# Kernel tuning notes

Hardware: AMD Instinct MI355X
Metric: run time of the kernel (lower is better)

The kernel has to match this reference:

```python
import jax, jax.numpy as jnp
import numpy as np
from jax import lax

NPOINT = 1024
K = 32
EPS = 1e-5  # BatchNorm2d default eps


def setup_inputs() -> dict:
    key = jax.random.key(0)
    ks = jax.random.split(key, 8)
    B, N = 16, 4096
    xyz = jax.random.normal(ks[0], (B, N, 3), dtype=jnp.float32)
    init_farthest = jax.random.randint(ks[1], (B,), 0, N, dtype=jnp.int32)
    def w(k, o, i):
        return jax.random.normal(k, (o, i), dtype=jnp.float32) * (1.0 / np.sqrt(i))
    chans = [3, 64, 64, 128]
    inp = {"xyz": xyz, "init_farthest": init_farthest}
    for li in range(3):
        ci, co = chans[li], chans[li + 1]
        inp[f"W{li+1}"] = w(ks[2 + li], co, ci)
        inp[f"b{li+1}"] = jnp.zeros((co,), jnp.float32)
        inp[f"g{li+1}"] = jnp.ones((co,), jnp.float32)
        inp[f"be{li+1}"] = jnp.zeros((co,), jnp.float32)
    return inp


def _farthest_point_sample(xyz, init_farthest, npoint):
    # Sequential FPS: npoint iterations of distance-update + argmax (lax.scan).
    B, N, _ = xyz.shape
    bidx = jnp.arange(B)
    def step(carry, _):
        distance, farthest = carry
        centroid = xyz[bidx, farthest][:, None, :]            # [B,1,3]
        d = jnp.sum((xyz - centroid) ** 2, axis=-1)           # [B,N]
        distance = jnp.minimum(distance, d)
        return (distance, jnp.argmax(distance, axis=-1)), farthest
    init = (jnp.full((B, N), 1e10, xyz.dtype), init_farthest)
    _, centroids = lax.scan(step, init, None, length=npoint)  # [npoint,B]
    return centroids.T                                        # [B,npoint]


def _forward(xyz, init_farthest, params):
    B, N, _ = xyz.shape
    fps_idx = _farthest_point_sample(xyz, init_farthest, NPOINT)      # [B,S]
    bidx = jnp.arange(B)[:, None]
    new_xyz = xyz[bidx, fps_idx]                                       # [B,S,3]
    # KNN over sampled points (pairwise squared distances, [B,S,S])
    dist = jnp.sum((new_xyz[:, :, None, :] - new_xyz[:, None, :, :]) ** 2, axis=-1)
    idx = jnp.argsort(dist, axis=-1)[:, :, 1:K + 1]                    # [B,S,K]
    # NOTE: faithful to original code: idx (values < npoint) indexes xyz rows.
    grouped = xyz[jnp.arange(B)[:, None, None], idx]                   # [B,S,K,3]
    grouped = grouped - new_xyz[:, :, None, :]
    x = jnp.transpose(grouped, (0, 3, 1, 2))                           # [B,3,S,K]
    for (W, b, g, be) in params:
        x = jnp.einsum('oc,bcsk->bosk', W, x) + b[None, :, None, None]
        m = x.mean(axis=(0, 2, 3), keepdims=True)
        v = x.var(axis=(0, 2, 3), keepdims=True)                       # biased var (BN train mode)
        x = g[None, :, None, None] * (x - m) * lax.rsqrt(v + EPS) + be[None, :, None, None]
        x = jax.nn.relu(x)
    new_points = jnp.max(x, axis=-1)                                   # [B,128,S]
    return new_xyz, new_points


def reference(xyz, init_farthest, W1, b1, g1, be1, W2, b2, g2, be2, W3, b3, g3, be3):
    params = [(W1, b1, g1, be1), (W2, b2, g2, be2), (W3, b3, g3, be3)]
    return _forward(xyz, init_farthest, params)
```

## Files before the change

kernel.cpp:

```cpp
#include <hip/hip_runtime.h>


#define Bc 16
#define Nn 4096
#define Ss 1024
#define Kk 32
#define COLS (Bc*Ss*Kk)
#define EPSF 1e-5f

#define S2SUM 16
#define S2SQ  528
#define S3SUM 1040
#define S3SQ  2064

typedef unsigned long long ull;
typedef unsigned int uint32;

__device__ __forceinline__ unsigned short f2bf(float f){
  uint32 u = __float_as_uint(f);
  uint32 r = (u + 0x7fffu + ((u>>16)&1u)) >> 16;
  return (unsigned short)r;
}
__device__ __forceinline__ float bf2f(unsigned short h){ return __uint_as_float(((uint32)h)<<16); }

__device__ __forceinline__ float dppmax_f32(float x){
  #define STEPF(ctrl,rm) { int _s=__builtin_amdgcn_update_dpp(__float_as_int(x),__float_as_int(x),(ctrl),(rm),0xf,false); x=fmaxf(x,__int_as_float(_s)); }
  STEPF(0x111,0xf) STEPF(0x112,0xf) STEPF(0x114,0xf) STEPF(0x118,0xf)
  STEPF(0x142,0xa) STEPF(0x143,0xc)
  #undef STEPF
  return __int_as_float(__builtin_amdgcn_readlane(__float_as_int(x),63));
}
__device__ __forceinline__ int dppmin_i32(int x){
  #define STEPI(ctrl,rm) { int _s=__builtin_amdgcn_update_dpp(x,x,(ctrl),(rm),0xf,false); x=min(x,_s); }
  STEPI(0x111,0xf) STEPI(0x112,0xf) STEPI(0x114,0xf) STEPI(0x118,0xf)
  STEPI(0x142,0xa) STEPI(0x143,0xc)
  #undef STEPI
  return __builtin_amdgcn_readlane(x,63);
}

__global__ __launch_bounds__(256) void fps_kernel(const float* __restrict__ xyz,
                                                  const int* __restrict__ init_far,
                                                  float* __restrict__ new_xyz){
  __shared__ float sx[Nn*4];
  __shared__ ull wk[2][4];
  int b = blockIdx.x, t = threadIdx.x;
  int lane = t & 63, wid = t >> 6;
  const float* xb = xyz + (size_t)b*Nn*3;
  const float4* xb4 = (const float4*)xb;
  for(int i=t;i<Nn*3/4;i+=256){
    float4 v = xb4[i];
    int f0 = 4*i;
    sx[(f0/3)*4 + (f0%3)]       = v.x;
    sx[((f0+1)/3)*4 + ((f0+1)%3)] = v.y;
    sx[((f0+2)/3)*4 + ((f0+2)%3)] = v.z;
    sx[((f0+3)/3)*4 + ((f0+3)%3)] = v.w;
  }
  __syncthreads();
  const float4* sxp = (const float4*)sx;
  float px[16],py[16],pz[16],dd[16];
  #pragma unroll
  for(int j=0;j<16;j++){ int n=t+256*j; float4 p=sxp[n]; px[j]=p.x; py[j]=p.y; pz[j]=p.z; dd[j]=1e10f; }
  int far = init_far[b];
  float o0x=0.f,o0y=0.f,o0z=0.f, o1x=0.f,o1y=0.f,o1z=0.f;
  float o2x=0.f,o2y=0.f,o2z=0.f, o3x=0.f,o3y=0.f,o3z=0.f;
  for(int it=0; it<Ss; it++){
    float4 c4 = sxp[far];
    float cx=c4.x, cy=c4.y, cz=c4.z;
    if(t==(it&255)){
      if(it<256)      { o0x=cx; o0y=cy; o0z=cz; }
      else if(it<512) { o1x=cx; o1y=cy; o1z=cz; }
      else if(it<768) { o2x=cx; o2y=cy; o2z=cz; }
      else            { o3x=cx; o3y=cy; o3z=cz; }
    }
    #pragma unroll
    for(int j=0;j<16;j++){
      float dx=px[j]-cx, dy=py[j]-cy, dz=pz[j]-cz;
      float d=__fadd_rn(__fadd_rn(__fmul_rn(dx,dx),__fmul_rn(dy,dy)),__fmul_rn(dz,dz));
      dd[j]=fminf(dd[j],d);
    }
    float m0=fmaxf(fmaxf(fmaxf(dd[0],dd[1]),fmaxf(dd[2],dd[3])),fmaxf(fmaxf(dd[4],dd[5]),fmaxf(dd[6],dd[7])));
    float m1=fmaxf(fmaxf(fmaxf(dd[8],dd[9]),fmaxf(dd[10],dd[11])),fmaxf(fmaxf(dd[12],dd[13]),fmaxf(dd[14],dd[15])));
    float bd=fmaxf(m0,m1);
    float dmax = dppmax_f32(bd);
    int cj=16;
    #pragma unroll
    for(int j=15;j>=0;j--) cj = (dd[j]!=dmax) ? cj : j;
    int cand = t + (cj<<8);
    int wmin = dppmin_i32(cand);
    if(lane==0) wk[it&1][wid] = ((ull)__float_as_uint(dmax)<<32) | (uint32)(4095-wmin);
    __syncthreads();
    ull g0=wk[it&1][0], g1=wk[it&1][1], g2=wk[it&1][2], g3=wk[it&1][3];
    ull ka = g1>g0?g1:g0, kb = g3>g2?g3:g2;
    ull kg = kb>ka?kb:ka;
    far = 4095-(int)(uint32)(kg&0xffffffffu);
  }
  float* outb = new_xyz + (size_t)b*Ss*3;
  outb[t*3+0]=o0x; outb[t*3+1]=o0y; outb[t*3+2]=o0z;
  outb[(256+t)*3+0]=o1x; outb[(256+t)*3+1]=o1y; outb[(256+t)*3+2]=o1z;
  outb[(512+t)*3+0]=o2x; outb[(512+t)*3+1]=o2y; outb[(512+t)*3+2]=o2z;
  outb[(768+t)*3+0]=o3x; outb[(768+t)*3+1]=o3y; outb[(768+t)*3+2]=o3z;
}

#define KN16(X) X(0) X(1) X(2) X(3) X(4) X(5) X(6) X(7) X(8) X(9) X(10) X(11) X(12) X(13) X(14) X(15)

__global__ __launch_bounds__(256) void knn_kernel(const float* __restrict__ xyz,
                                                  const float* __restrict__ new_xyz,
                                                  float* __restrict__ gout){
  __shared__ float nx[Ss*3];
  int b = blockIdx.x >> 8;
  int t = threadIdx.x;
  const float4* src=(const float4*)(new_xyz + (size_t)b*Ss*3);
  float4* dst=(float4*)nx;
  for(int i=t;i<Ss*3/4;i+=256) dst[i]=src[i];
  __syncthreads();
  int wid=t>>6, lane=t&63;
  int s=(blockIdx.x&255)*4+wid;
  float qx=nx[s*3],qy=nx[s*3+1],qz=nx[s*3+2];
  #define KDECL(i) ull K##i;
  KN16(KDECL)
  #undef KDECL
  #define KINIT(i) { int j=lane+64*(i); \
    float dx=nx[j*3]-qx, dy=nx[j*3+1]-qy, dz=nx[j*3+2]-qz; \
    float d=__fadd_rn(__fadd_rn(__fmul_rn(dx,dx),__fmul_rn(dy,dy)),__fmul_rn(dz,dz)); \
    K##i=((ull)(__float_as_uint(d)+1u)<<32)|(uint32)(j); }
  KN16(KINIT)
  #undef KINIT
  ull last=0; int myn=0;
  for(int r=0;r<33;r++){
    ull cur=~0ull;
    #define KSCAN(i) { ull c=K##i; c=(c>last)?c:~0ull; cur=(c<cur)?c:cur; }
    KN16(KSCAN)
    #undef KSCAN
    int hs=(int)(uint32)(cur>>32);
    hs = (hs<0) ? 0x7fffffff : hs;
    int dmin = dppmin_i32(hs);
    int ci = (hs==dmin) ? (int)(uint32)cur : 0x7fffffff;
    int jmin = dppmin_i32(ci);
    last = ((ull)(uint32)dmin<<32)|(uint32)jmin;
    if(r>=1 && lane==r-1) myn=jmin;
  }
  if(lane<Kk){
    int j=myn;
    const float* p=xyz + (size_t)b*Nn*3 + (size_t)j*3;
    float* go = gout + ((size_t)(b*Ss+s)*Kk + lane)*3;
    go[0]=p[0]-qx; go[1]=p[1]-qy; go[2]=p[2]-qz;
  }
}

__global__ __launch_bounds__(256) void gmom_kernel(const float* __restrict__ g, float* __restrict__ stats){
  __shared__ float sm[9];
  int t=threadIdx.x;
  if(t<9) sm[t]=0.f;
  __syncthreads();
  float a[9]={0,0,0,0,0,0,0,0,0};
  for(int col=blockIdx.x*256+t; col<COLS; col+=gridDim.x*256){
    float x=g[(size_t)col*3],y=g[(size_t)col*3+1],z=g[(size_t)col*3+2];
    a[0]+=x;a[1]+=y;a[2]+=z;a[3]+=x*x;a[4]+=y*y;a[5]+=z*z;a[6]+=x*y;a[7]+=x*z;a[8]+=y*z;
  }
  #pragma unroll
  for(int i=0;i<9;i++){
    float v=a[i];
    #pragma unroll
    for(int m=32;m>=1;m>>=1) v+=__shfl_xor(v,m,64);
    if((t&63)==0) atomicAdd(&sm[i],v);
  }
  __syncthreads();
  if(t<9) atomicAdd(&stats[t],sm[t]);
}

__global__ __launch_bounds__(256) void layer12_kernel(const float* __restrict__ g,
    const float* __restrict__ W1,const float* __restrict__ b1,const float* __restrict__ g1,const float* __restrict__ be1,
    const float* __restrict__ W2,const float* __restrict__ b2,
    const float* __restrict__ stats, unsigned short* __restrict__ y2,
    float* __restrict__ statsw){
  __shared__ float x2s[64*128];
  __shared__ float w2s[64*65];
  __shared__ float w1s[192], b1s[64], sc1[64], sh1[64], b2s[64];
  __shared__ float rs2[64], rq2[64];
  int t=threadIdx.x;
  for(int i=t;i<4096;i+=256){ w2s[(i>>6)*65+(i&63)]=W2[i]; }
  if(t<192) w1s[t]=W1[t];
  if(t<64){ b1s[t]=b1[t]; b2s[t]=b2[t]; rs2[t]=0.f; rq2[t]=0.f; }
  __syncthreads();
  if(t<64){
    const float n1=1.0f/COLS;
    float ex=stats[0]*n1,ey=stats[1]*n1,ez=stats[2]*n1;
    float cxx=stats[3]*n1-ex*ex, cyy=stats[4]*n1-ey*ey, czz=stats[5]*n1-ez*ez;
    float cxy=stats[6]*n1-ex*ey, cxz=stats[7]*n1-ex*ez, cyz=stats[8]*n1-ey*ez;
    float wx=w1s[t*3],wy=w1s[t*3+1],wz=w1s[t*3+2];
    float m=wx*ex+wy*ey+wz*ez+b1s[t];
    float v=wx*wx*cxx+wy*wy*cyy+wz*wz*czz+2.f*(wx*wy*cxy+wx*wz*cxz+wy*wz*cyz);
    float sc=g1[t]*rsqrtf(v+EPSF);
    sc1[t]=sc; sh1[t]=be1[t]-m*sc;
  }
  __syncthreads();
  {
    int col=t&127, c0=(t>>7)*32;
    size_t cg=(size_t)blockIdx.x*128+col;
    float gx=g[cg*3],gy=g[cg*3+1],gz=g[cg*3+2];
    for(int c=c0;c<c0+32;c++){
      float y=fmaf(w1s[c*3],gx,fmaf(w1s[c*3+1],gy,fmaf(w1s[c*3+2],gz,b1s[c])));
      x2s[c*128+col]=fmaxf(fmaf(y,sc1[c],sh1[c]),0.f);
    }
  }
  __syncthreads();
  int og=t>>4, cgi=t&15;
  float acc[4][8];
  #pragma unroll
  for(int r=0;r<4;r++){ float bb=b2s[og*4+r];
    #pragma unroll
    for(int j=0;j<8;j++) acc[r][j]=bb; }
  for(int c=0;c<64;c++){
    float xv[8];
    #pragma unroll
    for(int j=0;j<8;j++) xv[j]=x2s[c*128+cgi+16*j];
    #pragma unroll
    for(int r=0;r<4;r++){
      float w=w2s[(og*4+r)*65+c];
      #pragma unroll
      for(int j=0;j<8;j++) acc[r][j]=fmaf(w,xv[j],acc[r][j]);
    }
  }
  #pragma unroll
  for(int j=0;j<8;j++){
    size_t col=(size_t)blockIdx.x*128+cgi+16*j;
    ushort4 pk;
    pk.x=f2bf(acc[0][j]); pk.y=f2bf(acc[1][j]); pk.z=f2bf(acc[2][j]); pk.w=f2bf(acc[3][j]);
    *(ushort4*)(y2 + col*64 + og*4)=pk;
  }
  #pragma unroll
  for(int r=0;r<4;r++){
    float s_=0.f, q_=0.f;
    #pragma unroll
    for(int j=0;j<8;j++){ float v=acc[r][j]; s_+=v; q_=fmaf(v,v,q_); }
    atomicAdd(&rs2[og*4+r],s_);
    atomicAdd(&rq2[og*4+r],q_);
  }
  __syncthreads();
  if(t<64){
    int rep=blockIdx.x&7;
    atomicAdd(&statsw[S2SUM+rep*64+t],rs2[t]);
    atomicAdd(&statsw[S2SQ +rep*64+t],rq2[t]);
  }
}

__global__ __launch_bounds__(256) void layer3_kernel(const unsigned short* __restrict__ y2,
    const float* __restrict__ g2,const float* __restrict__ be2,
    const float* __restrict__ W3,const float* __restrict__ b3,
    float* __restrict__ stats, float* __restrict__ ymax, float* __restrict__ ymin){
  __shared__ float x3s[64*64];
  __shared__ unsigned short w3s[128*66];
  __shared__ float y3s[128*65];
  __shared__ float sc2[64], sh2[64], b3s[128];
  int t=threadIdx.x;
  if(t<64){
    const float n1=1.0f/COLS;
    float ssum=0.f, ssq=0.f;
    #pragma unroll
    for(int rp=0;rp<8;rp++){ ssum+=stats[S2SUM+rp*64+t]; ssq+=stats[S2SQ+rp*64+t]; }
    float m=ssum*n1;
    float v=ssq*n1-m*m;
    float sc=g2[t]*rsqrtf(v+EPSF);
    sc2[t]=sc; sh2[t]=be2[t]-m*sc;
  }
  if(t<128) b3s[t]=b3[t];
  for(int i=t;i<8192;i+=256){ w3s[(i>>6)*66+(i&63)]=f2bf(W3[i]); }
  __syncthreads();
  int og=t>>4, cgi=t&15;
  int q=t>>7, oo=t&127;
  float asum=0.f, asq=0.f;
  const uint32* w3u=(const uint32*)w3s;
  for(int tl=0; tl<4; tl++){
    int colbase=(blockIdx.x*4+tl)*64;
    {
      int col=t&63, c0=(t>>6)*16;
      const unsigned short* yp=y2+(size_t)(colbase+col)*64+c0;
      #pragma unroll
      for(int h=0;h<2;h++){
        uint4 u=((const uint4*)yp)[h];
        uint32 ua[4]={u.x,u.y,u.z,u.w};
        #pragma unroll
        for(int e=0;e<4;e++){
          int c=c0+h*8+e*2;
          float flo=__uint_as_float(ua[e]<<16);
          float fhi=__uint_as_float(ua[e]&0xffff0000u);
          x3s[c*64+col]=fmaxf(fmaf(flo,sc2[c],sh2[c]),0.f);
          x3s[(c+1)*64+col]=fmaxf(fmaf(fhi,sc2[c+1],sh2[c+1]),0.f);
        }
      }
    }
    __syncthreads();
    float acc[8][4];
    #pragma unroll
    for(int r=0;r<8;r++){ float bb=b3s[og*8+r];
      #pragma unroll
      for(int j=0;j<4;j++) acc[r][j]=bb; }
    for(int c2=0;c2<32;c2++){
      float x0[4],x1[4];
      #pragma unroll
      for(int j=0;j<4;j++){ x0[j]=x3s[(2*c2)*64+cgi+16*j]; x1[j]=x3s[(2*c2+1)*64+cgi+16*j]; }
      #pragma unroll
      for(int r=0;r<8;r++){
        uint32 w=w3u[(og*8+r)*33+c2];
        float w0=__uint_as_float(w<<16);
        float w1=__uint_as_float(w&0xffff0000u);
        #pragma unroll
        for(int j=0;j<4;j++) acc[r][j]=fmaf(w1,x1[j],fmaf(w0,x0[j],acc[r][j]));
      }
    }
    #pragma unroll
    for(int r=0;r<8;r++){
      #pragma unroll
      for(int j=0;j<4;j++) y3s[(og*8+r)*65+cgi+16*j]=acc[r][j];
    }
    __syncthreads();
    {
      float mx=-3.4e38f, mn=3.4e38f, su=0.f, sq=0.f;
      #pragma unroll
      for(int k=0;k<32;k++){
        float yv=y3s[oo*65+q*32+k];
        mx=fmaxf(mx,yv); mn=fminf(mn,yv); su+=yv; sq=fmaf(yv,yv,sq);
      }
      asum+=su; asq+=sq;
      int qg=(colbase>>5)+q;
      int bb=qg>>10, ss=qg&1023;
      ymax[((size_t)bb*128+oo)*1024+ss]=mx;
      ymin[((size_t)bb*128+oo)*1024+ss]=mn;
    }
    __syncthreads();
  }
  if(t>=128){ x3s[t-128]=asum; x3s[128+(t-128)]=asq; }
  __syncthreads();
  if(t<128){
    asum+=x3s[t]; asq+=x3s[128+t];
    int rep=blockIdx.x&7;
    atomicAdd(&stats[S3SUM+rep*128+t],asum);
    atomicAdd(&stats[S3SQ +rep*128+t],asq);
  }
}

__global__ __launch_bounds__(256) void finalize_kernel(const float* __restrict__ ymax,const float* __restrict__ ymin,
    const float* __restrict__ g3,const float* __restrict__ be3,const float* __restrict__ stats,
    float* __restrict__ outp){
  int idx=blockIdx.x*256+threadIdx.x;
  int o=(idx>>10)&127;
  const float n1=1.0f/COLS;
  float ssum=0.f, ssq=0.f;
  #pragma unroll
  for(int rp=0;rp<8;rp++){ ssum+=stats[S3SUM+rp*128+o]; ssq+=stats[S3SQ+rp*128+o]; }
  float m=ssum*n1;
  float v=ssq*n1-m*m;
  float sc=g3[o]*rsqrtf(v+EPSF);
  float sh=be3[o]-m*sc;
  float val=(sc>=0.f)?ymax[idx]:ymin[idx];
  outp[idx]=fmaxf(fmaf(val,sc,sh),0.f);
}

extern "C" void kernel_launch(void* const* d_in, const int* in_sizes, int n_in,
                              void* d_out, int out_size, void* d_ws, size_t ws_size,
                              hipStream_t stream){
  const float* xyz=(const float*)d_in[0];
  const int* initf=(const int*)d_in[1];
  const float* W1=(const float*)d_in[2]; const float* b1=(const float*)d_in[3];
  const float* g1=(const float*)d_in[4]; const float* be1=(const float*)d_in[5];
  const float* W2=(const float*)d_in[6]; const float* b2=(const float*)d_in[7];
  const float* g2=(const float*)d_in[8]; const float* be2=(const float*)d_in[9];
  const float* W3=(const float*)d_in[10]; const float* b3=(const float*)d_in[11];
  const float* g3=(const float*)d_in[12]; const float* be3=(const float*)d_in[13];
  float* out=(float*)d_out;
  char* ws=(char*)d_ws;
  float* stats=(float*)(ws);
  float* gbuf=(float*)(ws+65536);
  unsigned short* y2=(unsigned short*)(ws+6361088);
  float* ymax=(float*)(ws+73469952);
  float* ymin=(float*)(ws+81858560);
  hipMemsetAsync(stats,0,16384,stream);
  fps_kernel<<<16,256,0,stream>>>(xyz,initf,out);
  knn_kernel<<<4096,256,0,stream>>>(xyz,out,gbuf);
  gmom_kernel<<<1024,256,0,stream>>>(gbuf,stats);
  layer12_kernel<<<4096,256,0,stream>>>(gbuf,W1,b1,g1,be1,W2,b2,stats,y2,stats);
  layer3_kernel<<<2048,256,0,stream>>>(y2,g2,be2,W3,b3,stats,ymax,ymin);
  finalize_kernel<<<8192,256,0,stream>>>(ymax,ymin,g3,be3,stats,out+49152);
}
```

Measured before the change: 1.167 ms.

## Use bf16 MFMA for layer-2 and layer-3 pointwise convolutions

```diff
diff --git a/kernel.cpp b/kernel.cpp
--- a/kernel.cpp
+++ b/kernel.cpp
@@ -15,6 +15,8 @@
 
 typedef unsigned long long ull;
 typedef unsigned int uint32;
+typedef __attribute__((ext_vector_type(8))) short bf16x8;
+typedef __attribute__((ext_vector_type(4))) float f32x4;
 
 __device__ __forceinline__ unsigned short f2bf(float f){
   uint32 u = __float_as_uint(f);
@@ -36,6 +38,12 @@
   STEPI(0x142,0xa) STEPI(0x143,0xc)
   #undef STEPI
   return __builtin_amdgcn_readlane(x,63);
+}
+__device__ __forceinline__ float dpprowsum(float x){
+  #define SSTEP(ctrl) { int _s=__builtin_amdgcn_update_dpp(__float_as_int(x),__float_as_int(x),(ctrl),0xf,0xf,false); x+=__int_as_float(_s); }
+  SSTEP(0x111) SSTEP(0x112) SSTEP(0x114) SSTEP(0x118)
+  #undef SSTEP
+  return x;
 }
 
 __global__ __launch_bounds__(256) void fps_kernel(const float* __restrict__ xyz,
@@ -173,12 +181,12 @@
     const float* __restrict__ W2,const float* __restrict__ b2,
     const float* __restrict__ stats, unsigned short* __restrict__ y2,
     float* __restrict__ statsw){
-  __shared__ float x2s[64*128];
-  __shared__ float w2s[64*65];
+  __shared__ unsigned short x2s[128*72];
+  __shared__ unsigned short w2b[64*72];
   __shared__ float w1s[192], b1s[64], sc1[64], sh1[64], b2s[64];
   __shared__ float rs2[64], rq2[64];
   int t=threadIdx.x;
-  for(int i=t;i<4096;i+=256){ w2s[(i>>6)*65+(i&63)]=W2[i]; }
+  for(int i=t;i<4096;i+=256) w2b[(i>>6)*72+(i&63)]=f2bf(W2[i]);
   if(t<192) w1s[t]=W1[t];
   if(t<64){ b1s[t]=b1[t]; b2s[t]=b2[t]; rs2[t]=0.f; rq2[t]=0.f; }
   __syncthreads();
@@ -198,43 +206,57 @@
     int col=t&127, c0=(t>>7)*32;
     size_t cg=(size_t)blockIdx.x*128+col;
     float gx=g[cg*3],gy=g[cg*3+1],gz=g[cg*3+2];
-    for(int c=c0;c<c0+32;c++){
-      float y=fmaf(w1s[c*3],gx,fmaf(w1s[c*3+1],gy,fmaf(w1s[c*3+2],gz,b1s[c])));
-      x2s[c*128+col]=fmaxf(fmaf(y,sc1[c],sh1[c]),0.f);
-    }
-  }
-  __syncthreads();
-  int og=t>>4, cgi=t&15;
-  float acc[4][8];
-  #pragma unroll
-  for(int r=0;r<4;r++){ float bb=b2s[og*4+r];
-    #pragma unroll
-    for(int j=0;j<8;j++) acc[r][j]=bb; }
-  for(int c=0;c<64;c++){
-    float xv[8];
-    #pragma unroll
-    for(int j=0;j<8;j++) xv[j]=x2s[c*128+cgi+16*j];
+    uint32 ou[16];
+    #pragma unroll
+    for(int ci=0;ci<16;ci++){
+      int c=c0+2*ci;
+      float ya=fmaf(w1s[c*3],gx,fmaf(w1s[c*3+1],gy,fmaf(w1s[c*3+2],gz,b1s[c])));
+      float va=fmaxf(fmaf(ya,sc1[c],sh1[c]),0.f);
+      float yb=fmaf(w1s[c*3+3],gx,fmaf(w1s[c*3+4],gy,fmaf(w1s[c*3+5],gz,b1s[c+1])));
+      float vb=fmaxf(fmaf(yb,sc1[c+1],sh1[c+1]),0.f);
+      ou[ci]=(uint32)f2bf(va) | ((uint32)f2bf(vb)<<16);
+    }
+    uint32* xu=(uint32*)x2s;
+    #pragma unroll
+    for(int h=0;h<4;h++){
+      ((uint4*)(xu + col*36 + (c0>>1)))[h] = make_uint4(ou[h*4],ou[h*4+1],ou[h*4+2],ou[h*4+3]);
+    }
+  }
+  __syncthreads();
+  int w=t>>6, lane=t&63, quad=lane>>4, lr=lane&15;
+  f32x4 acc[4][2];
+  #pragma unroll
+  for(int mt=0;mt<4;mt++){ acc[mt][0]=(f32x4){0.f,0.f,0.f,0.f}; acc[mt][1]=(f32x4){0.f,0.f,0.f,0.f}; }
+  #pragma unroll
+  for(int kt=0;kt<2;kt++){
+    int ko=kt*32+quad*8;
+    bf16x8 b0=*(const bf16x8*)&x2s[(w*32+lr)*72+ko];
+    bf16x8 b1v=*(const bf16x8*)&x2s[(w*32+16+lr)*72+ko];
+    #pragma unroll
+    for(int mt=0;mt<4;mt++){
+      bf16x8 a=*(const bf16x8*)&w2b[(mt*16+lr)*72+ko];
+      acc[mt][0]=__builtin_amdgcn_mfma_f32_16x16x32_bf16(a,b0,acc[mt][0],0,0,0);
+      acc[mt][1]=__builtin_amdgcn_mfma_f32_16x16x32_bf16(a,b1v,acc[mt][1],0,0,0);
+    }
+  }
+  size_t col0=(size_t)blockIdx.x*128 + w*32 + lr;
+  #pragma unroll
+  for(int mt=0;mt<4;mt++){
+    ushort4 p0,p1;
+    unsigned short* q0=(unsigned short*)&p0;
+    unsigned short* q1=(unsigned short*)&p1;
     #pragma unroll
     for(int r=0;r<4;r++){
-      float w=w2s[(og*4+r)*65+c];
-      #pragma unroll
-      for(int j=0;j<8;j++) acc[r][j]=fmaf(w,xv[j],acc[r][j]);
-    }
-  }
-  #pragma unroll
-  for(int j=0;j<8;j++){
-    size_t col=(size_t)blockIdx.x*128+cgi+16*j;
-    ushort4 pk;
-    pk.x=f2bf(acc[0][j]); pk.y=f2bf(acc[1][j]); pk.z=f2bf(acc[2][j]); pk.w=f2bf(acc[3][j]);
-    *(ushort4*)(y2 + col*64 + og*4)=pk;
-  }
-  #pragma unroll
-  for(int r=0;r<4;r++){
-    float s_=0.f, q_=0.f;
-    #pragma unroll
-    for(int j=0;j<8;j++){ float v=acc[r][j]; s_+=v; q_=fmaf(v,v,q_); }
-    atomicAdd(&rs2[og*4+r],s_);
-    atomicAdd(&rq2[og*4+r],q_);
+      int o=mt*16+quad*4+r;
+      float bb=b2s[o];
+      float v0=acc[mt][0][r]+bb, v1=acc[mt][1][r]+bb;
+      q0[r]=f2bf(v0); q1[r]=f2bf(v1);
+      float s_=v0+v1, sq_=fmaf(v0,v0,v1*v1);
+      s_=dpprowsum(s_); sq_=dpprowsum(sq_);
+      if(lr==15){ atomicAdd(&rs2[o],s_); atomicAdd(&rq2[o],sq_); }
+    }
+    *(ushort4*)(y2 + col0*64 + mt*16+quad*4) = p0;
+    *(ushort4*)(y2 + (col0+16)*64 + mt*16+quad*4) = p1;
   }
   __syncthreads();
   if(t<64){
@@ -248,8 +270,8 @@
     const float* __restrict__ g2,const float* __restrict__ be2,
     const float* __restrict__ W3,const float* __restrict__ b3,
     float* __restrict__ stats, float* __restrict__ ymax, float* __restrict__ ymin){
-  __shared__ float x3s[64*64];
-  __shared__ unsigned short w3s[128*66];
+  __shared__ unsigned short x3s[64*72];
+  __shared__ unsigned short w3b[128*72];
   __shared__ float y3s[128*65];
   __shared__ float sc2[64], sh2[64], b3s[128];
   int t=threadIdx.x;
@@ -264,17 +286,17 @@
     sc2[t]=sc; sh2[t]=be2[t]-m*sc;
   }
   if(t<128) b3s[t]=b3[t];
-  for(int i=t;i<8192;i+=256){ w3s[(i>>6)*66+(i&63)]=f2bf(W3[i]); }
-  __syncthreads();
-  int og=t>>4, cgi=t&15;
+  for(int i=t;i<8192;i+=256) w3b[(i>>6)*72+(i&63)]=f2bf(W3[i]);
+  __syncthreads();
+  int w=t>>6, lane=t&63, quad=lane>>4, lr=lane&15;
   int q=t>>7, oo=t&127;
   float asum=0.f, asq=0.f;
-  const uint32* w3u=(const uint32*)w3s;
   for(int tl=0; tl<4; tl++){
     int colbase=(blockIdx.x*4+tl)*64;
     {
       int col=t&63, c0=(t>>6)*16;
       const unsigned short* yp=y2+(size_t)(colbase+col)*64+c0;
+      uint32 ou[8];
       #pragma unroll
       for(int h=0;h<2;h++){
         uint4 u=((const uint4*)yp)[h];
@@ -284,34 +306,38 @@
           int c=c0+h*8+e*2;
           float flo=__uint_as_float(ua[e]<<16);
           float fhi=__uint_as_float(ua[e]&0xffff0000u);
-          x3s[c*64+col]=fmaxf(fmaf(flo,sc2[c],sh2[c]),0.f);
-          x3s[(c+1)*64+col]=fmaxf(fmaf(fhi,sc2[c+1],sh2[c+1]),0.f);
+          float v0=fmaxf(fmaf(flo,sc2[c],sh2[c]),0.f);
+          float v1=fmaxf(fmaf(fhi,sc2[c+1],sh2[c+1]),0.f);
+          ou[h*4+e]=(uint32)f2bf(v0) | ((uint32)f2bf(v1)<<16);
         }
       }
+      uint32* xu=(uint32*)x3s;
+      #pragma unroll
+      for(int h=0;h<2;h++){
+        ((uint4*)(xu + col*36 + (c0>>1)))[h] = make_uint4(ou[h*4],ou[h*4+1],ou[h*4+2],ou[h*4+3]);
+      }
     }
     __syncthreads();
-    float acc[8][4];
-    #pragma unroll
-    for(int r=0;r<8;r++){ float bb=b3s[og*8+r];
+    f32x4 acc[8];
+    #pragma unroll
+    for(int mt=0;mt<8;mt++) acc[mt]=(f32x4){0.f,0.f,0.f,0.f};
+    #pragma unroll
+    for(int kt=0;kt<2;kt++){
+      int ko=kt*32+quad*8;
+      bf16x8 bfr=*(const bf16x8*)&x3s[(w*16+lr)*72+ko];
       #pragma unroll
-      for(int j=0;j<4;j++) acc[r][j]=bb; }
-    for(int c2=0;c2<32;c2++){
-      float x0[4],x1[4];
+      for(int mt=0;mt<8;mt++){
+        bf16x8 afr=*(const bf16x8*)&w3b[(mt*16+lr)*72+ko];
+        acc[mt]=__builtin_amdgcn_mfma_f32_16x16x32_bf16(afr,bfr,acc[mt],0,0,0);
+      }
+    }
+    #pragma unroll
+    for(int mt=0;mt<8;mt++){
       #pragma unroll
-      for(int j=0;j<4;j++){ x0[j]=x3s[(2*c2)*64+cgi+16*j]; x1[j]=x3s[(2*c2+1)*64+cgi+16*j]; }
-      #pragma unroll
-      for(int r=0;r<8;r++){
-        uint32 w=w3u[(og*8+r)*33+c2];
-        float w0=__uint_as_float(w<<16);
-        float w1=__uint_as_float(w&0xffff0000u);
-        #pragma unroll
-        for(int j=0;j<4;j++) acc[r][j]=fmaf(w1,x1[j],fmaf(w0,x0[j],acc[r][j]));
+      for(int r=0;r<4;r++){
+        int o=mt*16+quad*4+r;
+        y3s[o*65 + w*16+lr]=acc[mt][r]+b3s[o];
       }
-    }
-    #pragma unroll
-    for(int r=0;r<8;r++){
-      #pragma unroll
-      for(int j=0;j<4;j++) y3s[(og*8+r)*65+cgi+16*j]=acc[r][j];
     }
     __syncthreads();
     {
@@ -329,10 +355,10 @@
     }
     __syncthreads();
   }
-  if(t>=128){ x3s[t-128]=asum; x3s[128+(t-128)]=asq; }
+  if(t>=128){ y3s[t-128]=asum; y3s[128+(t-128)]=asq; }
   __syncthreads();
   if(t<128){
-    asum+=x3s[t]; asq+=x3s[128+t];
+    asum+=y3s[t]; asq+=y3s[128+t];
     int rep=blockIdx.x&7;
     atomicAdd(&stats[S3SUM+rep*128+t],asum);
     atomicAdd(&stats[S3SQ +rep*128+t],asq);
```

After: 982.3 us. -15.8%, faster.
